# Kernel optimization log

Hardware: AMD Instinct MI355X
Metric: run time of the kernel (lower is better)

Reference implementation:

```python
import jax, jax.numpy as jnp
import numpy as np


def setup_inputs() -> dict:
    key = jax.random.key(0)
    k1, k2 = jax.random.split(key)
    B, G, P = 64, 4999, 50
    raw_gene_expr = jax.random.normal(k1, (B, G), dtype=jnp.float32)
    # binary pathway membership matrix, mimics torch.randint(0, 2, (P, G)).float()
    pathway_gene_matrix = (jax.random.uniform(k2, (P, G)) < 0.5).astype(jnp.float32)
    return {"raw_gene_expr": raw_gene_expr, "pathway_gene_matrix": pathway_gene_matrix}


def reference(raw_gene_expr, pathway_gene_matrix):
    """Vectorized ssGSEA enrichment (compute_pathway_activations0).

    raw_gene_expr:        [B, G] float
    pathway_gene_matrix:  [P, G] binary float
    returns:              [B, P] signed max-deviation enrichment scores
    """
    B, G = raw_gene_expr.shape
    P = pathway_gene_matrix.shape[0]

    # Sort genes per sample in descending expression order
    order = jnp.argsort(-raw_gene_expr, axis=1)                      # [B, G]
    sorted_expr = jnp.take_along_axis(raw_gene_expr, order, axis=1)  # [B, G]

    # hit[b, p, i] = 1 if gene at sorted position i belongs to pathway p
    hit = (pathway_gene_matrix[:, order] > 0)                        # [P, B, G]
    hit = jnp.transpose(hit, (1, 0, 2)).astype(raw_gene_expr.dtype)  # [B, P, G]

    size = jnp.sum(pathway_gene_matrix > 0, axis=1).astype(raw_gene_expr.dtype)  # [P]

    # Weighted hit increments: |expr|^0.25 over hits, normalized per (sample, pathway)
    w = (jnp.abs(sorted_expr) ** 0.25)[:, None, :] * hit             # [B, P, G]
    s = jnp.sum(w, axis=-1, keepdims=True)
    w = jnp.where(s > 0, w / jnp.where(s > 0, s, 1.0), w)

    cum_hit = jnp.cumsum(w, axis=-1)                                 # [B, P, G]
    denom = jnp.maximum(G - size, 1.0)[None, :, None]                # guard size==G
    cum_miss = jnp.cumsum((1.0 - hit) / denom, axis=-1)              # [B, P, G]

    running = cum_hit - cum_miss                                     # [B, P, G]
    pos = jnp.argmax(jnp.abs(running), axis=-1)                      # [B, P]
    # signed max deviation == running value at the argmax of |running|
    es = jnp.take_along_axis(running, pos[..., None], axis=-1)[..., 0]  # [B, P]
    es = jnp.where(size[None, :] > 0, es, 0.0)
    return es
```

## Files before the change

### kernel.cpp

```cpp
#include <hip/hip_runtime.h>
#include <math.h>

typedef unsigned long long ull;

constexpr int Bc = 64;
constexpr int Gc = 4999;
constexpr int Pc = 50;

constexpr int RUN   = 1024;
constexpr int NRUN  = 5;
constexpr int NPAD  = NRUN * RUN;
constexpr int LPW4  = 21;
constexpr int QSPAN = 64 * LPW4;
constexpr ull PADKEY = 0xFFFFFFFFFFFFFFFFull;

__device__ __forceinline__ ull shfl_xor64(ull v, int lm) {
    int lo = __shfl_xor((int)(unsigned)(v & 0xFFFFFFFFull), lm, 64);
    int hi = __shfl_xor((int)(unsigned)(v >> 32), lm, 64);
    return ((ull)(unsigned)hi << 32) | (unsigned)lo;
}

__global__ __launch_bounds__(512) void chunk_sort(
    const float* __restrict__ expr, const float* __restrict__ pathway,
    ull* __restrict__ runs, ull* __restrict__ pbits, int P, int G)
{
    __shared__ ull key[RUN];
    const int r = blockIdx.x, b = blockIdx.y, tid = threadIdx.x;
    const int base = tid * 2;
    const float* row = expr + (size_t)b * G;

    ull v[2];
#pragma unroll
    for (int o = 0; o < 2; ++o) {
        int i = r * RUN + base + o;
        if (i < G) {
            unsigned u = __float_as_uint(row[i]);
            unsigned m = (u >> 31) ? ~u : (u | 0x80000000u);
            v[o] = ((ull)(~m) << 32) | (unsigned)i;
        } else {
            v[o] = PADKEY;
        }
    }

    for (int kk = 2; kk <= RUN; kk <<= 1) {
        const int j0 = kk >> 1;
        if (j0 >= 128) {
#pragma unroll
            for (int o = 0; o < 2; ++o) key[base + o] = v[o];
            __syncthreads();
            for (int j = j0; j >= 128; j >>= 1) {
                for (int t = tid; t < RUN / 2; t += 512) {
                    int i  = ((t & ~(j - 1)) << 1) | (t & (j - 1));
                    int ix = i | j;
                    ull a = key[i], c = key[ix];
                    bool up = ((i & kk) == 0);
                    if ((a > c) == up) { key[i] = c; key[ix] = a; }
                }
                __syncthreads();
            }
#pragma unroll
            for (int o = 0; o < 2; ++o) v[o] = key[base + o];
        }
        int jstart = (j0 > 64) ? 64 : j0;
        for (int j = jstart; j >= 2; j >>= 1) {
            int lm = j >> 1;
            bool takeMin = (((tid & lm) == 0) == ((base & kk) == 0));
#pragma unroll
            for (int o = 0; o < 2; ++o) {
                ull c = shfl_xor64(v[o], lm);
                ull mn = (v[o] < c) ? v[o] : c;
                ull mx = (v[o] < c) ? c : v[o];
                v[o] = takeMin ? mn : mx;
            }
        }
        {
            bool up = ((base & kk) == 0);
            if ((v[0] > v[1]) == up) { ull t = v[0]; v[0] = v[1]; v[1] = t; }
        }
    }

    ull* dst = runs + ((size_t)b * NRUN + r) * RUN;
#pragma unroll
    for (int o = 0; o < 2; ++o) dst[base + o] = v[o];

    if (r == 0) {
        int g = b * 512 + tid;
        if (g < G) {
            ull m = 0;
#pragma unroll
            for (int p = 0; p < Pc; ++p)
                if (pathway[(size_t)p * G + g] > 0.0f) m |= (1ull << p);
            pbits[g] = m;
        }
    }
}

__global__ __launch_bounds__(1024) void rank_scatter(
    const ull* __restrict__ runs, const ull* __restrict__ pbits,
    float* __restrict__ wqout, ull* __restrict__ pbout, int G)
{
    __shared__ ull runsLDS[NPAD];
    const int rg = blockIdx.x, b = blockIdx.y, tid = threadIdx.x;

    const ull* rowruns = runs + (size_t)b * NPAD;
    for (int i = tid; i < NPAD; i += 1024) runsLDS[i] = rowruns[i];
    __syncthreads();

    const int e = rg * 1024 + tid;
    const ull keyv = runsLDS[e];
    if (keyv == PADKEY) return;

    const int idx = (int)(unsigned)(keyv & 0xFFFFFFFFu);
    const ull pb = pbits[idx];

    const int run = e >> 10;
    int rank = e & 1023;
#pragma unroll
    for (int rr = 0; rr < NRUN; ++rr) {
        if (rr == run) continue;
        const ull* arr = &runsLDS[rr * RUN];
        int pos = 0;
#pragma unroll
        for (int s = RUN; s >= 1; s >>= 1) {
            int np = pos + s;
            if (np <= RUN && arr[np - 1] < keyv) pos = np;
        }
        rank += pos;
    }

    unsigned m = ~((unsigned)(keyv >> 32));
    unsigned absbits = ((m >> 31) ? m : ~m) & 0x7FFFFFFFu;
    float av = __uint_as_float(absbits);
    wqout[(size_t)b * G + rank] = sqrtf(sqrtf(av));
    pbout[(size_t)b * G + rank] = pb;
}

__global__ __launch_bounds__(1024) void es_kernel(
    const float* __restrict__ wq, const ull* __restrict__ pb64,
    float* __restrict__ out, int B, int P, int G)
{
    __shared__ float    swq[Gc];
    __shared__ unsigned sm32[Gc];
    __shared__ double   cSW[4][4][4];
    __shared__ int      cSH[4][4][4];
    __shared__ double   cBV[4][4][4];
    __shared__ double   cBR[4][4][4];

    const int pg = blockIdx.x;
    const int b  = blockIdx.y;
    const int tid = threadIdx.x;
    const int pbeg = pg * 13;
    const int pend = (pbeg + 13 < P) ? (pbeg + 13) : P;

    for (int i = tid; i < G; i += 1024) {
        swq[i]  = wq[(size_t)b * G + i];
        sm32[i] = (unsigned)(pb64[(size_t)b * G + i] >> pbeg);
    }
    __syncthreads();

    const int lane = tid & 63;
    const int w  = tid >> 6;
    const int qg = w >> 2;
    const int h  = w & 3;
    const int sh4 = qg * 4;

    const int lg = h * 64 + lane;
    const int start = lg * LPW4;
    int cnt = G - start;
    cnt = (cnt < 0) ? 0 : ((cnt > LPW4) ? LPW4 : cnt);

    double sw[4] = {0.0, 0.0, 0.0, 0.0};
    int sh[4] = {0, 0, 0, 0};
    for (int k = 0; k < cnt; ++k) {
        int s = start + k;
        unsigned nib = (sm32[s] >> sh4) & 15u;
        double wv = (double)swq[s];
#pragma unroll
        for (int q = 0; q < 4; ++q) {
            if ((nib >> q) & 1u) { sw[q] += wv; sh[q]++; }
        }
    }
#pragma unroll
    for (int q = 0; q < 4; ++q) {
        double s_ = sw[q]; int c_ = sh[q];
#pragma unroll
        for (int off = 1; off < 64; off <<= 1) {
            s_ += __shfl_xor(s_, off, 64);
            c_ += __shfl_xor(c_, off, 64);
        }
        if (lane == 0) { cSW[qg][h][q] = s_; cSH[qg][h][q] = c_; }
    }
    __syncthreads();

    int Qc[4];
#pragma unroll
    for (int hh = 0; hh < 4; ++hh) {
        int c = G - hh * QSPAN;
        Qc[hh] = (c < 0) ? 0 : ((c > QSPAN) ? QSPAN : c);
    }

    double norm[4], inv_denom[4], running[4];
    int shtot[4];
#pragma unroll
    for (int q = 0; q < 4; ++q) {
        double st = 0.0; int ct = 0;
#pragma unroll
        for (int hh = 0; hh < 4; ++hh) { st += cSW[qg][hh][q]; ct += cSH[qg][hh][q]; }
        shtot[q]     = ct;
        norm[q]      = (st > 0.0) ? 1.0 / st : 1.0;
        inv_denom[q] = 1.0 / fmax((double)(G - ct), 1.0);
        double offq = 0.0;
        for (int hh = 0; hh < h; ++hh)
            offq += cSW[qg][hh][q] * norm[q]
                  - (double)(Qc[hh] - cSH[qg][hh][q]) * inv_denom[q];
        double csum = sw[q] * norm[q] - (double)(cnt - sh[q]) * inv_denom[q];
        double x = csum;
#pragma unroll
        for (int off = 1; off < 64; off <<= 1) {
            double vv = __shfl_up(x, off, 64);
            if (lane >= off) x += vv;
        }
        running[q] = x - csum + offq;
    }

    double bestv[4] = {-1.0, -1.0, -1.0, -1.0};
    double bestr[4] = {0.0, 0.0, 0.0, 0.0};
    int besti[4] = {0x7FFFFFFF, 0x7FFFFFFF, 0x7FFFFFFF, 0x7FFFFFFF};
    for (int k = 0; k < cnt; ++k) {
        int s = start + k;
        unsigned nib = (sm32[s] >> sh4) & 15u;
        double wv = (double)swq[s];
#pragma unroll
        for (int q = 0; q < 4; ++q) {
            running[q] += ((nib >> q) & 1u) ? wv * norm[q] : -inv_denom[q];
            double a = fabs(running[q]);
            if (a > bestv[q]) { bestv[q] = a; bestr[q] = running[q]; besti[q] = s; }
        }
    }
#pragma unroll
    for (int q = 0; q < 4; ++q) {
#pragma unroll
        for (int off = 1; off < 64; off <<= 1) {
            double ov  = __shfl_xor(bestv[q], off, 64);
            double orr = __shfl_xor(bestr[q], off, 64);
            int    oi  = __shfl_xor(besti[q], off, 64);
            if (ov > bestv[q] || (ov == bestv[q] && oi < besti[q])) {
                bestv[q] = ov; bestr[q] = orr; besti[q] = oi;
            }
        }
        if (lane == 0) { cBV[qg][h][q] = bestv[q]; cBR[qg][h][q] = bestr[q]; }
    }
    __syncthreads();

    if (h == 0 && lane == 0) {
#pragma unroll
        for (int q = 0; q < 4; ++q) {
            double bv = cBV[qg][0][q];
            double br = cBR[qg][0][q];
#pragma unroll
            for (int hh = 1; hh < 4; ++hh) {
                double v_ = cBV[qg][hh][q];
                if (v_ > bv) { bv = v_; br = cBR[qg][hh][q]; }
            }
            int p = pbeg + sh4 + q;
            if (p < pend)
                out[(size_t)b * P + p] = (shtot[q] > 0) ? (float)br : 0.0f;
        }
    }
}

extern "C" void kernel_launch(void* const* d_in, const int* in_sizes, int n_in,
                              void* d_out, int out_size, void* d_ws, size_t ws_size,
                              hipStream_t stream) {
    const float* expr    = (const float*)d_in[0];
    const float* pathway = (const float*)d_in[1];
    float* out = (float*)d_out;

    char* ws = (char*)d_ws;
    ull*   pbits = (ull*)ws;
    ull*   runs  = (ull*)(ws + 40960);
    float* wqa   = (float*)(ws + 2662400);
    ull*   pb64  = (ull*)(ws + 3942144);

    chunk_sort<<<dim3(NRUN, Bc), dim3(512), 0, stream>>>(
        expr, pathway, runs, pbits, Pc, Gc);
    rank_scatter<<<dim3(NRUN, Bc), dim3(1024), 0, stream>>>(runs, pbits, wqa, pb64, Gc);
    es_kernel<<<dim3(4, Bc), dim3(1024), 0, stream>>>(
        wqa, pb64, out, Bc, Pc, Gc);
}
```

Measured before the change: 105.5 us.

## Widen sort per-thread work, interleave scatter output, unroll padded ES scan

chunk_sort now runs 256 threads holding 4 keys each, so more bitonic stages are done in registers and fewer go through shared-memory passes. rank_scatter writes weight and pathway bits as one interleaved 16-byte record instead of two separate arrays, and es_kernel reads that record. es_kernel pads shared memory to a multiple of the per-lane span so both scan loops become fixed-length and fully unrolled. It also defers the per-pathway normalization to a single final multiply, which removes one multiply per step from the inner loop. Pad entries are marked as zero-weight hits and their count is subtracted afterwards, which adds bookkeeping and slightly changes floating-point rounding.

```diff
diff --git a/kernel.cpp b/kernel.cpp
--- a/kernel.cpp
+++ b/kernel.cpp
@@ -11,6 +11,7 @@
 constexpr int NRUN  = 5;
 constexpr int NPAD  = NRUN * RUN;
 constexpr int LPW4  = 21;
+constexpr int PADG  = 256 * LPW4;
 constexpr int QSPAN = 64 * LPW4;
 constexpr ull PADKEY = 0xFFFFFFFFFFFFFFFFull;
 
@@ -20,18 +21,18 @@
     return ((ull)(unsigned)hi << 32) | (unsigned)lo;
 }
 
-__global__ __launch_bounds__(512) void chunk_sort(
+__global__ __launch_bounds__(256) void chunk_sort(
     const float* __restrict__ expr, const float* __restrict__ pathway,
     ull* __restrict__ runs, ull* __restrict__ pbits, int P, int G)
 {
     __shared__ ull key[RUN];
     const int r = blockIdx.x, b = blockIdx.y, tid = threadIdx.x;
-    const int base = tid * 2;
+    const int base = tid * 4;
     const float* row = expr + (size_t)b * G;
 
-    ull v[2];
-#pragma unroll
-    for (int o = 0; o < 2; ++o) {
+    ull v[4];
+#pragma unroll
+    for (int o = 0; o < 4; ++o) {
         int i = r * RUN + base + o;
         if (i < G) {
             unsigned u = __float_as_uint(row[i]);
@@ -44,12 +45,13 @@
 
     for (int kk = 2; kk <= RUN; kk <<= 1) {
         const int j0 = kk >> 1;
-        if (j0 >= 128) {
-#pragma unroll
-            for (int o = 0; o < 2; ++o) key[base + o] = v[o];
+        if (j0 >= 256) {
+#pragma unroll
+            for (int o = 0; o < 4; ++o) key[base + o] = v[o];
             __syncthreads();
-            for (int j = j0; j >= 128; j >>= 1) {
-                for (int t = tid; t < RUN / 2; t += 512) {
+            for (int j = j0; j >= 256; j >>= 1) {
+#pragma unroll
+                for (int t = tid; t < RUN / 2; t += 256) {
                     int i  = ((t & ~(j - 1)) << 1) | (t & (j - 1));
                     int ix = i | j;
                     ull a = key[i], c = key[ix];
@@ -59,32 +61,41 @@
                 __syncthreads();
             }
 #pragma unroll
-            for (int o = 0; o < 2; ++o) v[o] = key[base + o];
-        }
-        int jstart = (j0 > 64) ? 64 : j0;
-        for (int j = jstart; j >= 2; j >>= 1) {
-            int lm = j >> 1;
+            for (int o = 0; o < 4; ++o) v[o] = key[base + o];
+        }
+        int jstart = (j0 > 128) ? 128 : j0;
+        for (int j = jstart; j >= 4; j >>= 1) {
+            int lm = j >> 2;
             bool takeMin = (((tid & lm) == 0) == ((base & kk) == 0));
 #pragma unroll
-            for (int o = 0; o < 2; ++o) {
+            for (int o = 0; o < 4; ++o) {
                 ull c = shfl_xor64(v[o], lm);
                 ull mn = (v[o] < c) ? v[o] : c;
                 ull mx = (v[o] < c) ? c : v[o];
                 v[o] = takeMin ? mn : mx;
             }
         }
-        {
-            bool up = ((base & kk) == 0);
-            if ((v[0] > v[1]) == up) { ull t = v[0]; v[0] = v[1]; v[1] = t; }
+#pragma unroll
+        for (int j = 2; j >= 1; j >>= 1) {
+            if (j < kk) {
+#pragma unroll
+                for (int o = 0; o < 4; ++o) {
+                    if ((o & j) == 0) {
+                        bool up = (((base + o) & kk) == 0);
+                        ull a = v[o], c = v[o | j];
+                        if ((a > c) == up) { v[o] = c; v[o | j] = a; }
+                    }
+                }
+            }
         }
     }
 
     ull* dst = runs + ((size_t)b * NRUN + r) * RUN;
 #pragma unroll
-    for (int o = 0; o < 2; ++o) dst[base + o] = v[o];
+    for (int o = 0; o < 4; ++o) dst[base + o] = v[o];
 
     if (r == 0) {
-        int g = b * 512 + tid;
+        int g = b * 256 + tid;
         if (g < G) {
             ull m = 0;
 #pragma unroll
@@ -97,7 +108,7 @@
 
 __global__ __launch_bounds__(1024) void rank_scatter(
     const ull* __restrict__ runs, const ull* __restrict__ pbits,
-    float* __restrict__ wqout, ull* __restrict__ pbout, int G)
+    ulonglong2* __restrict__ wp, int G)
 {
     __shared__ ull runsLDS[NPAD];
     const int rg = blockIdx.x, b = blockIdx.y, tid = threadIdx.x;
@@ -131,16 +142,18 @@
     unsigned m = ~((unsigned)(keyv >> 32));
     unsigned absbits = ((m >> 31) ? m : ~m) & 0x7FFFFFFFu;
     float av = __uint_as_float(absbits);
-    wqout[(size_t)b * G + rank] = sqrtf(sqrtf(av));
-    pbout[(size_t)b * G + rank] = pb;
+    ulonglong2 t;
+    t.x = pb;
+    t.y = (ull)__float_as_uint(sqrtf(sqrtf(av)));
+    wp[(size_t)b * G + rank] = t;
 }
 
 __global__ __launch_bounds__(1024) void es_kernel(
-    const float* __restrict__ wq, const ull* __restrict__ pb64,
-    float* __restrict__ out, int B, int P, int G)
+    const ulonglong2* __restrict__ wp, float* __restrict__ out,
+    int B, int P, int G)
 {
-    __shared__ float    swq[Gc];
-    __shared__ unsigned sm32[Gc];
+    __shared__ float    swq[PADG];
+    __shared__ unsigned sm32[PADG];
     __shared__ double   cSW[4][4][4];
     __shared__ int      cSH[4][4][4];
     __shared__ double   cBV[4][4][4];
@@ -152,9 +165,15 @@
     const int pbeg = pg * 13;
     const int pend = (pbeg + 13 < P) ? (pbeg + 13) : P;
 
-    for (int i = tid; i < G; i += 1024) {
-        swq[i]  = wq[(size_t)b * G + i];
-        sm32[i] = (unsigned)(pb64[(size_t)b * G + i] >> pbeg);
+    for (int i = tid; i < PADG; i += 1024) {
+        if (i < G) {
+            ulonglong2 t = wp[(size_t)b * G + i];
+            swq[i]  = __uint_as_float((unsigned)t.y);
+            sm32[i] = (unsigned)(t.x >> pbeg);
+        } else {
+            swq[i]  = 0.0f;
+            sm32[i] = 0xFFFFFFFFu;
+        }
     }
     __syncthreads();
 
@@ -166,23 +185,24 @@
 
     const int lg = h * 64 + lane;
     const int start = lg * LPW4;
-    int cnt = G - start;
-    cnt = (cnt < 0) ? 0 : ((cnt > LPW4) ? LPW4 : cnt);
+    int npads = start + LPW4 - G;
+    npads = (npads < 0) ? 0 : ((npads > LPW4) ? LPW4 : npads);
 
     double sw[4] = {0.0, 0.0, 0.0, 0.0};
-    int sh[4] = {0, 0, 0, 0};
-    for (int k = 0; k < cnt; ++k) {
+    int shl[4] = {0, 0, 0, 0};
+#pragma unroll
+    for (int k = 0; k < LPW4; ++k) {
         int s = start + k;
-        unsigned nib = (sm32[s] >> sh4) & 15u;
+        unsigned b4 = sm32[s] >> sh4;
         double wv = (double)swq[s];
 #pragma unroll
         for (int q = 0; q < 4; ++q) {
-            if ((nib >> q) & 1u) { sw[q] += wv; sh[q]++; }
+            if ((b4 >> q) & 1u) { sw[q] += wv; shl[q]++; }
         }
     }
 #pragma unroll
     for (int q = 0; q < 4; ++q) {
-        double s_ = sw[q]; int c_ = sh[q];
+        double s_ = sw[q]; int c_ = shl[q] - npads;
 #pragma unroll
         for (int off = 1; off < 64; off <<= 1) {
             s_ += __shfl_xor(s_, off, 64);
@@ -199,42 +219,44 @@
         Qc[hh] = (c < 0) ? 0 : ((c > QSPAN) ? QSPAN : c);
     }
 
-    double norm[4], inv_denom[4], running[4];
+    double negE[4], normq[4], runn[4];
     int shtot[4];
 #pragma unroll
     for (int q = 0; q < 4; ++q) {
         double st = 0.0; int ct = 0;
 #pragma unroll
         for (int hh = 0; hh < 4; ++hh) { st += cSW[qg][hh][q]; ct += cSH[qg][hh][q]; }
-        shtot[q]     = ct;
-        norm[q]      = (st > 0.0) ? 1.0 / st : 1.0;
-        inv_denom[q] = 1.0 / fmax((double)(G - ct), 1.0);
+        shtot[q] = ct;
+        double d = 1.0 / fmax((double)(G - ct), 1.0);
+        double e = (st > 0.0) ? d * st : d;
+        negE[q]  = -e;
+        normq[q] = (st > 0.0) ? 1.0 / st : 1.0;
         double offq = 0.0;
         for (int hh = 0; hh < h; ++hh)
-            offq += cSW[qg][hh][q] * norm[q]
-                  - (double)(Qc[hh] - cSH[qg][hh][q]) * inv_denom[q];
-        double csum = sw[q] * norm[q] - (double)(cnt - sh[q]) * inv_denom[q];
+            offq += cSW[qg][hh][q] - (double)(Qc[hh] - cSH[qg][hh][q]) * e;
+        double csum = sw[q] - (double)(LPW4 - shl[q]) * e;
         double x = csum;
 #pragma unroll
         for (int off = 1; off < 64; off <<= 1) {
             double vv = __shfl_up(x, off, 64);
             if (lane >= off) x += vv;
         }
-        running[q] = x - csum + offq;
+        runn[q] = x - csum + offq;
     }
 
     double bestv[4] = {-1.0, -1.0, -1.0, -1.0};
     double bestr[4] = {0.0, 0.0, 0.0, 0.0};
     int besti[4] = {0x7FFFFFFF, 0x7FFFFFFF, 0x7FFFFFFF, 0x7FFFFFFF};
-    for (int k = 0; k < cnt; ++k) {
+#pragma unroll
+    for (int k = 0; k < LPW4; ++k) {
         int s = start + k;
-        unsigned nib = (sm32[s] >> sh4) & 15u;
+        unsigned b4 = sm32[s] >> sh4;
         double wv = (double)swq[s];
 #pragma unroll
         for (int q = 0; q < 4; ++q) {
-            running[q] += ((nib >> q) & 1u) ? wv * norm[q] : -inv_denom[q];
-            double a = fabs(running[q]);
-            if (a > bestv[q]) { bestv[q] = a; bestr[q] = running[q]; besti[q] = s; }
+            runn[q] += ((b4 >> q) & 1u) ? wv : negE[q];
+            double a = fabs(runn[q]);
+            if (a > bestv[q]) { bestv[q] = a; bestr[q] = runn[q]; besti[q] = s; }
         }
     }
 #pragma unroll
@@ -264,7 +286,8 @@
             }
             int p = pbeg + sh4 + q;
             if (p < pend)
-                out[(size_t)b * P + p] = (shtot[q] > 0) ? (float)br : 0.0f;
+                out[(size_t)b * P + p] =
+                    (shtot[q] > 0) ? (float)(br * normq[q]) : 0.0f;
         }
     }
 }
@@ -277,14 +300,13 @@
     float* out = (float*)d_out;
 
     char* ws = (char*)d_ws;
-    ull*   pbits = (ull*)ws;
-    ull*   runs  = (ull*)(ws + 40960);
-    float* wqa   = (float*)(ws + 2662400);
-    ull*   pb64  = (ull*)(ws + 3942144);
-
-    chunk_sort<<<dim3(NRUN, Bc), dim3(512), 0, stream>>>(
+    ull*        pbits = (ull*)ws;
+    ull*        runs  = (ull*)(ws + 40960);
+    ulonglong2* wp    = (ulonglong2*)(ws + 2662400);
+
+    chunk_sort<<<dim3(NRUN, Bc), dim3(256), 0, stream>>>(
         expr, pathway, runs, pbits, Pc, Gc);
-    rank_scatter<<<dim3(NRUN, Bc), dim3(1024), 0, stream>>>(runs, pbits, wqa, pb64, Gc);
+    rank_scatter<<<dim3(NRUN, Bc), dim3(1024), 0, stream>>>(runs, pbits, wp, Gc);
     es_kernel<<<dim3(4, Bc), dim3(1024), 0, stream>>>(
-        wqa, pb64, out, Bc, Pc, Gc);
-}
+        wp, out, Bc, Pc, Gc);
+}
```

Result: no change. 103.9 us (-1.5%).
